# Performance work log

Hardware: AMD Instinct MI355X
Metric: run time of the kernel (lower is better)

## Reference

```python
import jax, jax.numpy as jnp
import numpy as np

MODEL_DIM = 512
NUM_HEADS = 8
HEAD_DIM = 64
INNER = NUM_HEADS * HEAD_DIM  # 512 == MODEL_DIM -> projection is Identity


def setup_inputs() -> dict:
    key = jax.random.key(0)
    ks = jax.random.split(key, 7)
    B, T = 2, 4096
    x = jax.random.normal(ks[0], (B, T, MODEL_DIM), dtype=jnp.float32)
    s = 1.0 / np.sqrt(MODEL_DIM)
    Wq = jax.random.normal(ks[1], (MODEL_DIM, INNER), dtype=jnp.float32) * s
    Wk = jax.random.normal(ks[2], (MODEL_DIM, INNER), dtype=jnp.float32) * s
    Wv = jax.random.normal(ks[3], (MODEL_DIM, INNER), dtype=jnp.float32) * s
    bq = jax.random.normal(ks[4], (INNER,), dtype=jnp.float32) * 0.01
    bk = jax.random.normal(ks[5], (INNER,), dtype=jnp.float32) * 0.01
    bv = jax.random.normal(ks[6], (INNER,), dtype=jnp.float32) * 0.01
    return {"x": x, "Wq": Wq, "bq": bq, "Wk": Wk, "bk": bk, "Wv": Wv, "bv": bv}


def reference(x, Wq, bq, Wk, bk, Wv, bv):
    B, T, _ = x.shape
    # project and split heads: [B, H, T, D]
    q = (x @ Wq + bq).reshape(B, T, NUM_HEADS, HEAD_DIM).transpose(0, 2, 1, 3)
    k = (x @ Wk + bk).reshape(B, T, NUM_HEADS, HEAD_DIM).transpose(0, 2, 1, 3)
    v = (x @ Wv + bv).reshape(B, T, NUM_HEADS, HEAD_DIM).transpose(0, 2, 1, 3)
    scale = 1.0 / np.sqrt(HEAD_DIM).astype(np.float32)
    attn = jnp.einsum('bhqd,bhkd->bhqk', q, k) * scale  # [B,H,Tq,Tkv]
    attn = jax.nn.softmax(attn, axis=-1)
    out = jnp.einsum('bhqk,bhkd->bhqd', attn, v)        # [B,H,Tq,D]
    out = out.transpose(0, 2, 1, 3).reshape(B, T, INNER)
    return out  # projection is Identity since INNER == MODEL_DIM
```

## Files before the change

### kernel.cpp

```cpp
#include <hip/hip_runtime.h>
#include <hip/hip_bf16.h>


typedef __attribute__((ext_vector_type(8)))  _Float16 half8;
typedef __attribute__((ext_vector_type(2)))  __fp16   fp16x2;
typedef __attribute__((ext_vector_type(4)))  float    f32x4;
typedef __attribute__((ext_vector_type(16))) float    f32x16;

#define TSEQ 4096
#define DH   64
#define NH   8
#define MD   512

#if __has_builtin(__builtin_amdgcn_exp2f)
__device__ inline float fexp2(float x){ return __builtin_amdgcn_exp2f(x); }
#else
__device__ inline float fexp2(float x){ float r; asm("v_exp_f32 %0, %1\n\ts_nop 1" : "=v"(r) : "v"(x)); return r; }
#endif

union H2U { fp16x2 h; unsigned int u; };
__device__ inline unsigned int pkrtz(float a, float b){
  H2U c; c.h = __builtin_amdgcn_cvt_pkrtz(a, b); return c.u;
}

union U4H8 { uint4 u; half8 h; };

#define AS3U(p) ((__attribute__((address_space(3))) unsigned int*)(p))
#define AS1U(p) ((const __attribute__((address_space(1))) unsigned int*)(p))

__global__ __launch_bounds__(256) void k_conv_x(const float* __restrict__ x, _Float16* __restrict__ xh){
  int i = (blockIdx.x*256 + threadIdx.x)*8;
  float4 a = *(const float4*)(x+i);
  float4 b = *(const float4*)(x+i+4);
  half8 o;
  o[0]=(_Float16)a.x; o[1]=(_Float16)a.y; o[2]=(_Float16)a.z; o[3]=(_Float16)a.w;
  o[4]=(_Float16)b.x; o[5]=(_Float16)b.y; o[6]=(_Float16)b.z; o[7]=(_Float16)b.w;
  *(half8*)(xh+i) = o;
}

__global__ __launch_bounds__(256) void k_prep_w(const float* __restrict__ Wq, const float* __restrict__ Wk,
                                                const float* __restrict__ Wv, _Float16* __restrict__ wt){
  __shared__ float tile[32][33];
  const int mat = blockIdx.z;
  const float* W = mat==0 ? Wq : (mat==1 ? Wk : Wv);
  const int n0 = blockIdx.x*32, k0 = blockIdx.y*32;
  const int tx = threadIdx.x & 31, ty = threadIdx.x >> 5;
  #pragma unroll
  for (int i=0;i<4;i++){ int k = ty*4+i; tile[k][tx] = W[(size_t)(k0+k)*MD + n0 + tx]; }
  __syncthreads();
  _Float16* dst = wt + (size_t)mat*MD*MD;
  #pragma unroll
  for (int i=0;i<4;i++){ int n = ty*4+i; dst[(size_t)(n0+n)*MD + k0 + tx] = (_Float16)tile[tx][n]; }
}

__global__ __launch_bounds__(256,2) void k_qkv(const _Float16* __restrict__ xh, const _Float16* __restrict__ wt,
              const float* __restrict__ bq, const float* __restrict__ bk, const float* __restrict__ bv,
              _Float16* __restrict__ qout, _Float16* __restrict__ kout, _Float16* __restrict__ vout){
  __shared__ alignas(16) _Float16 Ash[2][128*64];
  __shared__ alignas(16) _Float16 Bsh[2][128*64];
  const int tid = threadIdx.x, w = tid>>6, l = tid&63;
  const int fr = l&15, hi = l>>4;
  const int nt = blockIdx.x, mt = blockIdx.y;
  const int mat = nt>>2;
  const int n0  = (nt&3)*128;
  const int m0  = mt*128;
  const _Float16* W = wt + (size_t)mat*MD*MD;
  const int wr = (w>>1)*64, wc = (w&1)*64;

  f32x4 acc[4][4];
  #pragma unroll
  for (int a=0;a<4;a++)
    #pragma unroll
    for (int b=0;b<4;b++) acc[a][b] = (f32x4){0.f,0.f,0.f,0.f};

#define QSTAGE(k0_, buf) do { \
    _Pragma("unroll") \
    for (int i_=0;i_<4;i_++){ \
      int slot_ = tid + i_*256; \
      int row_ = slot_>>3, seg_ = (slot_&7) ^ (row_&7); \
      __builtin_amdgcn_global_load_lds(AS1U(xh + (size_t)(m0+row_)*MD + (k0_) + seg_*8), \
          AS3U((char*)&Ash[buf][0] + slot_*16), 16, 0, 0); \
      __builtin_amdgcn_global_load_lds(AS1U(W + (size_t)(n0+row_)*MD + (k0_) + seg_*8), \
          AS3U((char*)&Bsh[buf][0] + slot_*16), 16, 0, 0); \
    } \
  } while(0)

  QSTAGE(0, 0);

  for (int ks0=0; ks0<8; ks0++){
    const int cur = ks0&1;
    __syncthreads();
    if (ks0+1 < 8) QSTAGE((ks0+1)*64, cur^1);
    const _Float16* Ab = &Ash[cur][0];
    const _Float16* Bb = &Bsh[cur][0];
    #pragma unroll
    for (int ks=0;ks<2;ks++){
      half8 af[4], bfr[4];
      #pragma unroll
      for (int mi=0;mi<4;mi++){
        int row = wr + mi*16 + fr;
        af[mi] = *(const half8*)&Ab[row*64 + (((ks*4+hi) ^ (row&7))<<3)];
      }
      #pragma unroll
      for (int ni=0;ni<4;ni++){
        int row = wc + ni*16 + fr;
        bfr[ni] = *(const half8*)&Bb[row*64 + (((ks*4+hi) ^ (row&7))<<3)];
      }
      #pragma unroll
      for (int mi=0;mi<4;mi++)
        #pragma unroll
        for (int ni=0;ni<4;ni++)
          acc[mi][ni] = __builtin_amdgcn_mfma_f32_16x16x32_f16(af[mi], bfr[ni], acc[mi][ni], 0,0,0);
    }
  }
#undef QSTAGE

  const float* bias = mat==0 ? bq : (mat==1 ? bk : bv);
  const float scl = (mat==0) ? 0.125f*1.4426950408889634f : (mat==2 ? 0.0625f : 1.0f);
  if (mat==1){
    #pragma unroll
    for (int ni=0;ni<4;ni++){
      int n_in = n0 + wc + ni*16 + fr;
      float bb = bias[n_in];
      int h = n_in>>6, d = n_in&63;
      #pragma unroll
      for (int mi=0;mi<4;mi++)
        #pragma unroll
        for (int r=0;r<4;r++){
          int m = m0 + wr + mi*16 + hi*4 + r;
          float v = acc[mi][ni][r] + bb;
          int b_ = m>>12, t = m&4095;
          kout[ ((((size_t)(b_*NH + h))*8 + (d>>3))*TSEQ + t)*8 + (d&7) ] = (_Float16)v;
        }
    }
  } else {
    _Float16* dst = mat==0 ? qout : vout;
    #pragma unroll
    for (int ni=0;ni<4;ni++){
      int n_in = n0 + wc + ni*16 + fr;
      float bb = bias[n_in];
      int h = n_in>>6, d = n_in&63;
      #pragma unroll
      for (int mi=0;mi<4;mi++)
        #pragma unroll
        for (int r=0;r<4;r++){
          int m = m0 + wr + mi*16 + hi*4 + r;
          float v = (acc[mi][ni][r] + bb)*scl;
          int b_ = m>>12, t = m&4095;
          dst[ ((size_t)((b_*NH + h)*TSEQ + t))*DH + d ] = (_Float16)v;
        }
    }
  }
}

__global__ __launch_bounds__(256) void k_trans_v(const _Float16* __restrict__ v, _Float16* __restrict__ vtg){
  __shared__ _Float16 tile[64][72];
  const int tid = threadIdx.x;
  const int bh = blockIdx.y, t0 = blockIdx.x*64;
  const _Float16* src = v + ((size_t)bh*TSEQ + t0)*DH;
  #pragma unroll
  for (int i=0;i<2;i++){
    int slot = tid + i*256; int r = slot>>3, s = slot&7;
    *(half8*)&tile[r][s*8] = *(const half8*)(src + (size_t)r*DH + s*8);
  }
  __syncthreads();
  #pragma unroll
  for (int i=0;i<2;i++){
    int slot = tid + i*256;
    int d = slot&63, sg = slot>>6;
    half8 o;
    #pragma unroll
    for (int j=0;j<8;j++) o[j] = tile[sg*8+j][d];
    *(half8*)(vtg + (((size_t)bh*512 + (t0>>3) + sg)*64 + d)*8) = o;
  }
}

__global__ __launch_bounds__(256,4) void k_attn(const _Float16* __restrict__ qb_, const _Float16* __restrict__ ktg,
                                                const _Float16* __restrict__ vtg, float* __restrict__ out,
                                                _Float16* __restrict__ pb, float* __restrict__ ps){
  __shared__ alignas(16) _Float16 Ksh[2*4096];
  __shared__ alignas(16) _Float16 Vsh[2*4096];
  const int tid = threadIdx.x, w = tid>>6, l = tid&63;
  const int ln31 = l&31, lh = l>>5;

  const int bid = blockIdx.x;
  const int swz = ((bid&7)<<7) | (bid>>3);
  const int bh = swz>>6;
  const int qblk = (swz&63)>>1;
  const int half = swz&1;

  const _Float16* Q  = qb_ + (size_t)bh*TSEQ*DH;
  const _Float16* Kt = ktg + (size_t)bh*8*TSEQ*8;
  const _Float16* Vt = vtg + (size_t)bh*512*64*8;
  const int q0 = qblk*128 + w*32;

  half8 qf[4];
  #pragma unroll
  for (int ds=0;ds<4;ds++)
    qf[ds] = *(const half8*)(Q + (size_t)(q0 + ln31)*DH + ds*16 + lh*8);

  f32x16 of0, of1, sacc;
  #pragma unroll
  for (int r=0;r<16;r++){ of0[r]=0.f; of1[r]=0.f; sacc[r]=0.f; }
  const half8 onesv = {(_Float16)1,(_Float16)1,(_Float16)1,(_Float16)1,
                       (_Float16)1,(_Float16)1,(_Float16)1,(_Float16)1};

  const int base16 = lh*512 + ln31*8;

#define STAGE(kt, buf) do { \
    const int k0_ = (kt)*64; \
    _Pragma("unroll") \
    for (int i_=0;i_<2;i_++){ \
      int base_ = i_*256 + w*64; \
      int slot_ = base_ + l; \
      int krow_ = slot_&63, kseg_ = slot_>>6; \
      __builtin_amdgcn_global_load_lds(AS1U(Kt + ((size_t)kseg_*TSEQ + k0_ + krow_)*8), \
          AS3U((char*)Ksh + (buf)*8192 + base_*16), 16, 0, 0); \
      __builtin_amdgcn_global_load_lds(AS1U(Vt + ((size_t)(slot_ + k0_*8))*8), \
          AS3U((char*)Vsh + (buf)*8192 + base_*16), 16, 0, 0); \
    } \
  } while(0)

  const int kt0 = half*32;
  STAGE(kt0, 0);

  for (int it=0; it<32; it++){
    const int cur = it&1;
    __syncthreads();
    if (it+1 < 32) STAGE(kt0+it+1, cur^1);

    const _Float16* Kb = &Ksh[cur*4096];
    const _Float16* Vb = &Vsh[cur*4096];

    #pragma unroll
    for (int kbq=0; kbq<2; kbq++){
      f32x16 s;
      #pragma unroll
      for (int r=0;r<16;r++) s[r]=0.f;
      #pragma unroll
      for (int ds=0;ds<4;ds++){
        half8 kf = *(const half8*)&Kb[base16 + ds*1024 + kbq*256];
        s = __builtin_amdgcn_mfma_f32_32x32x16_f16(kf, qf[ds], s, 0,0,0);
      }

      unsigned int wv[8];
      #pragma unroll
      for (int c=0;c<4;c++){
        float e0 = fexp2(s[4*c+0]);
        float e1 = fexp2(s[4*c+1]);
        float e2 = fexp2(s[4*c+2]);
        float e3 = fexp2(s[4*c+3]);
        wv[2*c+0] = pkrtz(e0, e1);
        wv[2*c+1] = pkrtz(e2, e3);
      }

      #pragma unroll
      for (int e=0;e<2;e++){
        unsigned int word[4];
        #pragma unroll
        for (int i=0;i<2;i++){
          unsigned int w0 = wv[4*e + i];
          unsigned int w1 = wv[4*e + 2 + i];
          unsigned int exp_ = (lh==0) ? w1 : w0;
          unsigned int cross = (unsigned int)__shfl((int)exp_, l ^ 32);
          word[i]   = (lh==0) ? w0 : cross;
          word[2+i] = (lh==0) ? cross : w1;
        }
        U4H8 pf; pf.u.x=word[0]; pf.u.y=word[1]; pf.u.z=word[2]; pf.u.w=word[3];
        const int ea = kbq*2 + e;
        half8 v0 = *(const half8*)&Vb[base16 + ea*1024];
        half8 v1 = *(const half8*)&Vb[base16 + ea*1024 + 256];
        sacc = __builtin_amdgcn_mfma_f32_32x32x16_f16(onesv, pf.h, sacc, 0,0,0);
        of0 = __builtin_amdgcn_mfma_f32_32x32x16_f16(v0, pf.h, of0, 0,0,0);
        of1 = __builtin_amdgcn_mfma_f32_32x32x16_f16(v1, pf.h, of1, 0,0,0);
      }
    }
  }

  if (lh==0) ps[half*65536 + bh*TSEQ + q0 + ln31] = sacc[0];

  if (half==0){
    const int b_ = bh>>3, h = bh&7;
    float* o = out + ((size_t)(b_*TSEQ + q0 + ln31))*MD + h*DH;
    #pragma unroll
    for (int rr=0;rr<4;rr++){
      float4 o4 = { of0[4*rr+0], of0[4*rr+1], of0[4*rr+2], of0[4*rr+3] };
      *(float4*)(o + rr*8 + lh*4) = o4;
    }
    #pragma unroll
    for (int rr=0;rr<4;rr++){
      float4 o4 = { of1[4*rr+0], of1[4*rr+1], of1[4*rr+2], of1[4*rr+3] };
      *(float4*)(o + 32 + rr*8 + lh*4) = o4;
    }
  } else {
    _Float16* o = pb + ((size_t)bh*TSEQ + q0 + ln31)*DH;
    #pragma unroll
    for (int rr=0;rr<4;rr++){
      uint2 pk = { pkrtz(of0[4*rr+0], of0[4*rr+1]), pkrtz(of0[4*rr+2], of0[4*rr+3]) };
      *(uint2*)(o + rr*8 + lh*4) = pk;
    }
    #pragma unroll
    for (int rr=0;rr<4;rr++){
      uint2 pk = { pkrtz(of1[4*rr+0], of1[4*rr+1]), pkrtz(of1[4*rr+2], of1[4*rr+3]) };
      *(uint2*)(o + 32 + rr*8 + lh*4) = pk;
    }
  }
#undef STAGE
}

__global__ __launch_bounds__(256) void k_comb(float* __restrict__ out, const _Float16* __restrict__ pb,
                                              const float* __restrict__ ps){
  int idx = (blockIdx.x*256 + threadIdx.x)*8;
  int d0 = idx & 511, t = (idx>>9)&4095, b = idx>>21;
  int h = d0>>6, bh = b*NH + h;
  float sc = 16.0f / (ps[bh*TSEQ + t] + ps[65536 + bh*TSEQ + t]);
  float4 a0 = *(float4*)(out+idx);
  float4 a1 = *(float4*)(out+idx+4);
  half8 pv = *(const half8*)(pb + ((size_t)bh*TSEQ + t)*DH + (d0&63));
  float4 r0 = { (a0.x + (float)pv[0])*sc, (a0.y + (float)pv[1])*sc,
                (a0.z + (float)pv[2])*sc, (a0.w + (float)pv[3])*sc };
  float4 r1 = { (a1.x + (float)pv[4])*sc, (a1.y + (float)pv[5])*sc,
                (a1.z + (float)pv[6])*sc, (a1.w + (float)pv[7])*sc };
  *(float4*)(out+idx)   = r0;
  *(float4*)(out+idx+4) = r1;
}

extern "C" void kernel_launch(void* const* d_in, const int* in_sizes, int n_in,
                              void* d_out, int out_size, void* d_ws, size_t ws_size,
                              hipStream_t stream) {
  const float* x  = (const float*)d_in[0];
  const float* Wq = (const float*)d_in[1];
  const float* bq = (const float*)d_in[2];
  const float* Wk = (const float*)d_in[3];
  const float* bk = (const float*)d_in[4];
  const float* Wv = (const float*)d_in[5];
  const float* bv = (const float*)d_in[6];
  float* out = (float*)d_out;

  char* ws = (char*)d_ws;
  _Float16* xh = (_Float16*)(ws);
  _Float16* wt = (_Float16*)(ws + ((size_t)8<<20));
  _Float16* qb = (_Float16*)(ws + ((size_t)10<<20));
  _Float16* kb = (_Float16*)(ws + ((size_t)18<<20));
  _Float16* vb = (_Float16*)(ws + ((size_t)26<<20));
  _Float16* vt = xh;
  _Float16* pb = vb;
  float*    ps = (float*)(ws + ((size_t)8<<20));

  k_conv_x<<<2048, 256, 0, stream>>>(x, xh);
  k_prep_w<<<dim3(16,16,3), 256, 0, stream>>>(Wq, Wk, Wv, wt);
  k_qkv<<<dim3(12,64), 256, 0, stream>>>(xh, wt, bq, bk, bv, qb, kb, vb);
  k_trans_v<<<dim3(64,16), 256, 0, stream>>>(vb, vt);
  k_attn<<<1024, 256, 0, stream>>>(qb, kb, vt, out, pb, ps);
  k_comb<<<2048, 256, 0, stream>>>(out, pb, ps);
}
```

Measured before the change: 139.4 us.

## Load K tiles directly into registers with prefetch instead of staging through LDS

K fragments are now read straight from global memory into a register double-buffer (krg), prefetched one iteration ahead, and the K LDS staging buffer is dropped. Only V is still staged through LDS. This removes the LDS traffic and LDS footprint for K, but adds register pressure, so launch bounds drop from 4 to 3 blocks per SM. Every wave now reads K from global/L2 on its own rather than sharing it through LDS.

```diff
diff --git a/kernel.cpp b/kernel.cpp
--- a/kernel.cpp
+++ b/kernel.cpp
@@ -175,10 +175,9 @@
   }
 }
 
-__global__ __launch_bounds__(256,4) void k_attn(const _Float16* __restrict__ qb_, const _Float16* __restrict__ ktg,
+__global__ __launch_bounds__(256,3) void k_attn(const _Float16* __restrict__ qb_, const _Float16* __restrict__ ktg,
                                                 const _Float16* __restrict__ vtg, float* __restrict__ out,
                                                 _Float16* __restrict__ pb, float* __restrict__ ps){
-  __shared__ alignas(16) _Float16 Ksh[2*4096];
   __shared__ alignas(16) _Float16 Vsh[2*4096];
   const int tid = threadIdx.x, w = tid>>6, l = tid&63;
   const int ln31 = l&31, lh = l>>5;
@@ -193,6 +192,7 @@
   const _Float16* Kt = ktg + (size_t)bh*8*TSEQ*8;
   const _Float16* Vt = vtg + (size_t)bh*512*64*8;
   const int q0 = qblk*128 + w*32;
+  const int kt0 = half*32;
 
   half8 qf[4];
   #pragma unroll
@@ -205,76 +205,94 @@
   const half8 onesv = {(_Float16)1,(_Float16)1,(_Float16)1,(_Float16)1,
                        (_Float16)1,(_Float16)1,(_Float16)1,(_Float16)1};
 
-  const int base16 = lh*512 + ln31*8;
-
-#define STAGE(kt, buf) do { \
+  const int vbase = lh*512 + ln31*8;
+
+  const _Float16* kp = Kt + ((size_t)lh*TSEQ + (size_t)kt0*64 + ln31)*8;
+
+#define VSTAGE(kt, buf) do { \
     const int k0_ = (kt)*64; \
     _Pragma("unroll") \
     for (int i_=0;i_<2;i_++){ \
       int base_ = i_*256 + w*64; \
       int slot_ = base_ + l; \
-      int krow_ = slot_&63, kseg_ = slot_>>6; \
-      __builtin_amdgcn_global_load_lds(AS1U(Kt + ((size_t)kseg_*TSEQ + k0_ + krow_)*8), \
-          AS3U((char*)Ksh + (buf)*8192 + base_*16), 16, 0, 0); \
       __builtin_amdgcn_global_load_lds(AS1U(Vt + ((size_t)(slot_ + k0_*8))*8), \
           AS3U((char*)Vsh + (buf)*8192 + base_*16), 16, 0, 0); \
     } \
   } while(0)
 
-  const int kt0 = half*32;
-  STAGE(kt0, 0);
+#define SOFT_PV(s, EA0, Vb) do { \
+    unsigned int wv[8]; \
+    _Pragma("unroll") \
+    for (int c=0;c<4;c++){ \
+      float e0 = fexp2((s)[4*c+0]); \
+      float e1 = fexp2((s)[4*c+1]); \
+      float e2 = fexp2((s)[4*c+2]); \
+      float e3 = fexp2((s)[4*c+3]); \
+      wv[2*c+0] = pkrtz(e0, e1); \
+      wv[2*c+1] = pkrtz(e2, e3); \
+    } \
+    _Pragma("unroll") \
+    for (int e=0;e<2;e++){ \
+      unsigned int word[4]; \
+      _Pragma("unroll") \
+      for (int i=0;i<2;i++){ \
+        unsigned int w0 = wv[4*e + i]; \
+        unsigned int w1 = wv[4*e + 2 + i]; \
+        unsigned int exp_ = (lh==0) ? w1 : w0; \
+        unsigned int cross = (unsigned int)__shfl((int)exp_, l ^ 32); \
+        word[i]   = (lh==0) ? w0 : cross; \
+        word[2+i] = (lh==0) ? cross : w1; \
+      } \
+      U4H8 pf; pf.u.x=word[0]; pf.u.y=word[1]; pf.u.z=word[2]; pf.u.w=word[3]; \
+      const int ea = (EA0) + e; \
+      half8 v0 = *(const half8*)&(Vb)[vbase + ea*1024]; \
+      half8 v1 = *(const half8*)&(Vb)[vbase + ea*1024 + 256]; \
+      sacc = __builtin_amdgcn_mfma_f32_32x32x16_f16(onesv, pf.h, sacc, 0,0,0); \
+      of0 = __builtin_amdgcn_mfma_f32_32x32x16_f16(v0, pf.h, of0, 0,0,0); \
+      of1 = __builtin_amdgcn_mfma_f32_32x32x16_f16(v1, pf.h, of1, 0,0,0); \
+    } \
+  } while(0)
+
+  VSTAGE(kt0, 0);
+  half8 krg[8];
+  #pragma unroll
+  for (int ds=0;ds<4;ds++){
+    krg[ds]   = *(const half8*)(kp + (size_t)ds*TSEQ*16);
+    krg[4+ds] = *(const half8*)(kp + (size_t)ds*TSEQ*16 + 256);
+  }
 
   for (int it=0; it<32; it++){
     const int cur = it&1;
     __syncthreads();
-    if (it+1 < 32) STAGE(kt0+it+1, cur^1);
-
-    const _Float16* Kb = &Ksh[cur*4096];
+    if (it+1 < 32) VSTAGE(kt0+it+1, cur^1);
+
     const _Float16* Vb = &Vsh[cur*4096];
-
-    #pragma unroll
-    for (int kbq=0; kbq<2; kbq++){
-      f32x16 s;
-      #pragma unroll
-      for (int r=0;r<16;r++) s[r]=0.f;
-      #pragma unroll
-      for (int ds=0;ds<4;ds++){
-        half8 kf = *(const half8*)&Kb[base16 + ds*1024 + kbq*256];
-        s = __builtin_amdgcn_mfma_f32_32x32x16_f16(kf, qf[ds], s, 0,0,0);
-      }
-
-      unsigned int wv[8];
-      #pragma unroll
-      for (int c=0;c<4;c++){
-        float e0 = fexp2(s[4*c+0]);
-        float e1 = fexp2(s[4*c+1]);
-        float e2 = fexp2(s[4*c+2]);
-        float e3 = fexp2(s[4*c+3]);
-        wv[2*c+0] = pkrtz(e0, e1);
-        wv[2*c+1] = pkrtz(e2, e3);
-      }
-
-      #pragma unroll
-      for (int e=0;e<2;e++){
-        unsigned int word[4];
-        #pragma unroll
-        for (int i=0;i<2;i++){
-          unsigned int w0 = wv[4*e + i];
-          unsigned int w1 = wv[4*e + 2 + i];
-          unsigned int exp_ = (lh==0) ? w1 : w0;
-          unsigned int cross = (unsigned int)__shfl((int)exp_, l ^ 32);
-          word[i]   = (lh==0) ? w0 : cross;
-          word[2+i] = (lh==0) ? cross : w1;
-        }
-        U4H8 pf; pf.u.x=word[0]; pf.u.y=word[1]; pf.u.z=word[2]; pf.u.w=word[3];
-        const int ea = kbq*2 + e;
-        half8 v0 = *(const half8*)&Vb[base16 + ea*1024];
-        half8 v1 = *(const half8*)&Vb[base16 + ea*1024 + 256];
-        sacc = __builtin_amdgcn_mfma_f32_32x32x16_f16(onesv, pf.h, sacc, 0,0,0);
-        of0 = __builtin_amdgcn_mfma_f32_32x32x16_f16(v0, pf.h, of0, 0,0,0);
-        of1 = __builtin_amdgcn_mfma_f32_32x32x16_f16(v1, pf.h, of1, 0,0,0);
-      }
-    }
+    const _Float16* kpn = kp + (size_t)(it+1)*512;
+
+    f32x16 s;
+    #pragma unroll
+    for (int r=0;r<16;r++) s[r]=0.f;
+    #pragma unroll
+    for (int ds=0;ds<4;ds++)
+      s = __builtin_amdgcn_mfma_f32_32x32x16_f16(krg[ds], qf[ds], s, 0,0,0);
+    if (it+1 < 32){
+      #pragma unroll
+      for (int ds=0;ds<4;ds++)
+        krg[ds] = *(const half8*)(kpn + (size_t)ds*TSEQ*16);
+    }
+    SOFT_PV(s, 0, Vb);
+
+    #pragma unroll
+    for (int r=0;r<16;r++) s[r]=0.f;
+    #pragma unroll
+    for (int ds=0;ds<4;ds++)
+      s = __builtin_amdgcn_mfma_f32_32x32x16_f16(krg[4+ds], qf[ds], s, 0,0,0);
+    if (it+1 < 32){
+      #pragma unroll
+      for (int ds=0;ds<4;ds++)
+        krg[4+ds] = *(const half8*)(kpn + (size_t)ds*TSEQ*16 + 256);
+    }
+    SOFT_PV(s, 2, Vb);
   }
 
   if (lh==0) ps[half*65536 + bh*TSEQ + q0 + ln31] = sacc[0];
@@ -305,7 +323,8 @@
       *(uint2*)(o + 32 + rr*8 + lh*4) = pk;
     }
   }
-#undef STAGE
+#undef VSTAGE
+#undef SOFT_PV
 }
 
 __global__ __launch_bounds__(256) void k_comb(float* __restrict__ out, const _Float16* __restrict__ pb,
```

Result: slower. 143.7 us (+3.1%).
